# Performance work log

Measured on AMD Instinct MI355X. Metric: run time of the kernel, lower is better.

Reference implementation:

```python
import jax, jax.numpy as jnp
import numpy as np

B, S, E = 2, 2048, 1024
H = 1344            # hidden_dim = ceil(1.3*1024/64)*64
NH = 4              # mLSTM heads
DH = H // NH        # 336
K = 4               # causal conv kernel size
NPH = H // 4        # headwise proj heads (qkv_proj_blocksize=4)
PD = H // NPH       # per-head proj dim = 4
EPS = 1e-6


def setup_inputs() -> dict:
    key = jax.random.key(0)
    ks = jax.random.split(key, 10)
    s_in = jnp.sqrt(2.0 / (5 * E))    # small_init(E)
    s_pd = jnp.sqrt(2.0 / (5 * PD))   # small_init per-head dim
    return {
        "x": jax.random.normal(ks[0], (B, S, E), jnp.float32),
        "W_up": jax.random.normal(ks[1], (E, 2 * H), jnp.float32) * s_in,
        "conv_k": jax.random.normal(ks[2], (K, 1, H), jnp.float32) * jnp.sqrt(2.0 / K),  # depthwise, WIO layout
        "conv_b": jnp.zeros((H,), jnp.float32),
        "Wq": jax.random.normal(ks[3], (NPH, PD, PD), jnp.float32) * s_pd,
        "Wk": jax.random.normal(ks[4], (NPH, PD, PD), jnp.float32) * s_pd,
        "Wv": jax.random.normal(ks[5], (NPH, PD, PD), jnp.float32) * s_pd,
        "W_ig": jax.random.normal(ks[6], (3 * H, NH), jnp.float32) * 0.01,
        "b_ig": jax.random.normal(ks[7], (NH,), jnp.float32) * 0.1,
        "W_fg": jax.random.normal(ks[8], (3 * H, NH), jnp.float32) * 0.01,
        "b_fg": jnp.linspace(3.0, 6.0, NH, dtype=jnp.float32),
        "ln_w": jnp.ones((H,), jnp.float32),
        "skip": jnp.ones((H,), jnp.float32),
        "W_down": jax.random.normal(ks[9], (H, E), jnp.float32) * (2.0 / 12 / np.sqrt(H)),
    }


def _headwise(x, W):
    # LinearHeadwiseExpand: block-diagonal projection over NPH heads of size PD
    xh = x.reshape(B, S, NPH, PD)
    return jnp.einsum('bshd,hdo->bsho', xh, W).reshape(B, S, H)


def _mlstm_cell(q, k, v, ig, fg):
    # parallel stabilized mLSTM; q,k,v: (B,NH,S,DH); ig,fg: (B,NH,S)
    logf = jax.nn.log_sigmoid(fg)
    c = jnp.cumsum(logf, axis=-1)                         # (B,NH,S)
    logfmat = c[..., :, None] - c[..., None, :]           # (B,NH,S,S) cumulative forget decay
    mask = jnp.tril(jnp.ones((S, S), bool))               # causal mask
    log_D = jnp.where(mask, logfmat, -jnp.inf) + ig[..., None, :]
    m = jnp.max(log_D, axis=-1, keepdims=True)            # rowwise stabilizer
    D = jnp.exp(log_D - m)
    qk = jnp.einsum('bnsd,bntd->bnst', q, k) * (DH ** -0.5)
    C = qk * D
    n = jnp.maximum(jnp.abs(jnp.sum(C, axis=-1, keepdims=True)), jnp.exp(-m))
    return jnp.einsum('bnst,bntd->bnsd', C / (n + EPS), v)


def reference(x, W_up, conv_k, conv_b, Wq, Wk, Wv, W_ig, b_ig, W_fg, b_fg, ln_w, skip, W_down):
    x_inner = x @ W_up                                    # (B,S,2H)
    x_m, z = jnp.split(x_inner, 2, axis=-1)
    # depthwise causal conv1d
    xp = jnp.pad(x_m, ((0, 0), (K - 1, 0), (0, 0)))
    xc = jax.lax.conv_general_dilated(
        xp, conv_k, (1,), 'VALID',
        dimension_numbers=('NWC', 'WIO', 'NWC'),
        feature_group_count=H) + conv_b
    act = jax.nn.silu(xc)
    q = _headwise(act, Wq)
    k = _headwise(act, Wk)
    v = _headwise(x_m, Wv)
    gin = jnp.concatenate([q, k, v], axis=-1)             # (B,S,3H)
    ig = jnp.transpose(gin @ W_ig + b_ig, (0, 2, 1))      # (B,NH,S)
    fg = jnp.transpose(gin @ W_fg + b_fg, (0, 2, 1))
    qh = jnp.transpose(q.reshape(B, S, NH, DH), (0, 2, 1, 3))
    kh = jnp.transpose(k.reshape(B, S, NH, DH), (0, 2, 1, 3))
    vh = jnp.transpose(v.reshape(B, S, NH, DH), (0, 2, 1, 3))
    h = _mlstm_cell(qh, kh, vh, ig, fg)                   # (B,NH,S,DH)
    # multi-head layernorm (per-head groupnorm over DH, scale only)
    mu = jnp.mean(h, axis=-1, keepdims=True)
    var = jnp.var(h, axis=-1, keepdims=True)
    hn = (h - mu) * jax.lax.rsqrt(var + 1e-5) * ln_w.reshape(NH, 1, DH)
    h_out = jnp.transpose(hn, (0, 2, 1, 3)).reshape(B, S, H)
    h_state = (h_out + skip * act) * jax.nn.silu(z)
    return h_state @ W_down
```

## Files before the change

kernel.cpp:

```cpp
#include <hip/hip_runtime.h>
#include <cmath>

#define DI __device__ __forceinline__

constexpr int B_=2, S_=2048, E_=1024, H_=1344, NH_=4, DH_=336;
constexpr int BS_=B_*S_, H2_=2*H_;
constexpr int NG_=B_*NH_*S_;

constexpr size_t N_X=(size_t)BS_*E_;
constexpr size_t N_WUP=(size_t)E_*H2_;
constexpr size_t N_WDN=(size_t)H_*E_;
constexpr size_t N_BSH=(size_t)BS_*H_;
constexpr size_t N_BSH2=(size_t)BS_*H2_;
constexpr size_t N_WH=5376, N_WG=16128, N_CK=4*H_;

constexpr size_t O_IGB = 64;
constexpr size_t O_LOGF= O_IGB + NG_;
constexpr size_t O_AB  = O_LOGF+ NG_;
constexpr size_t O_MB  = O_AB  + NG_;
constexpr size_t O_MTB = O_MB  + NG_;
constexpr size_t O_CK  = O_MTB + NG_;
constexpr size_t O_CB  = O_CK  + N_CK;
constexpr size_t O_WQ  = O_CB  + H_;
constexpr size_t O_WK  = O_WQ  + N_WH;
constexpr size_t O_WV  = O_WK  + N_WH;
constexpr size_t O_WIG = O_WV  + N_WH;
constexpr size_t O_BIG = O_WIG + N_WG;
constexpr size_t O_WFG = O_BIG + 16;
constexpr size_t O_BFG = O_WFG + N_WG;
constexpr size_t O_LNW = O_BFG + 16;
constexpr size_t O_SKP = O_LNW + H_;
constexpr size_t O_FX  = O_SKP + H_;
constexpr size_t O_FWUP= O_FX  + N_X;
constexpr size_t O_FWDN= O_FWUP+ N_WUP;
constexpr size_t O_XIN = O_FWDN+ N_WDN;
constexpr size_t O_ACT = O_XIN + N_BSH2;
constexpr size_t O_QB  = O_ACT + N_BSH;
constexpr size_t O_KB  = O_QB  + N_BSH;
constexpr size_t O_VB  = O_KB  + N_BSH;
constexpr size_t O_HOUT= O_VB  + N_BSH;

constexpr size_t KSPLIT_SHORTS=(size_t)8*128*11*64*8;
constexpr size_t VT_SHORTS=(size_t)8*64*22*64*8;

typedef __attribute__((ext_vector_type(8))) short bf16x8;
typedef __attribute__((ext_vector_type(4))) float f32x4;

DI float bf2f(unsigned int u){union{unsigned int i;float f;}v;v.i=(u&0xffffu)<<16;return v.f;}
DI unsigned short f2bf(float f){union{float f;unsigned int i;}v;v.f=f;unsigned int x=v.i;
  return (unsigned short)((x+0x7fffu+((x>>16)&1u))>>16);}
DI float siluf(float x){return x/(1.f+expf(-x));}
DI float logsigf(float x){return (x>=0.f)?-log1pf(expf(-x)):x-log1pf(expf(x));}
DI void load4(const float* p, float* d){float4 v=*reinterpret_cast<const float4*>(p);
  d[0]=v.x;d[1]=v.y;d[2]=v.z;d[3]=v.w;}

__global__ __launch_bounds__(256) void detect_k(const unsigned short* __restrict__ xraw,
                                                int* __restrict__ flag){
  __shared__ int cnt_s;
  if(threadIdx.x==0) cnt_s=0;
  __syncthreads();
  int c=0;
  for(int i=threadIdx.x;i<2048;i+=256){
    const unsigned e=(xraw[i]>>7)&0xFFu;
    if(e>=0x90u) c++;
  }
  atomicAdd(&cnt_s,c);
  __syncthreads();
  if(threadIdx.x==0) *flag=(cnt_s>16)?0:1;
}

constexpr int CV0=5376, CV1=CV0+1344, CV2=CV1+5376, CV3=CV2+5376, CV4=CV3+5376,
              CV5=CV4+16128, CV6=CV5+4, CV7=CV6+16128, CV8=CV7+4,
              CV9=CV8+1344, CVT=CV9+1344;

__global__ __launch_bounds__(256) void prepAB_k(const void* __restrict__ xsrc,
    const void* __restrict__ wsrc, const int* __restrict__ flag,
    unsigned short* __restrict__ xhi, unsigned short* __restrict__ xlo,
    unsigned short* __restrict__ whi, unsigned short* __restrict__ wlo,
    const void* s2,const void* s3,const void* s4,const void* s5,const void* s6,
    const void* s7,const void* s8,const void* s9,const void* s10,const void* s11,
    const void* s12, float* __restrict__ ws){
  const int blk=blockIdx.x;
  const int fl=*flag;
  if(blk>=3392){
    const int i=(blk-3392)*256+threadIdx.x;
    if(i>=CVT) return;
    const void* src; int off; size_t dst;
    if(i<CV0){src=s2; off=i;      dst=O_CK +off;}
    else if(i<CV1){src=s3; off=i-CV0; dst=O_CB +off;}
    else if(i<CV2){src=s4; off=i-CV1; dst=O_WQ +off;}
    else if(i<CV3){src=s5; off=i-CV2; dst=O_WK +off;}
    else if(i<CV4){src=s6; off=i-CV3; dst=O_WV +off;}
    else if(i<CV5){src=s7; off=i-CV4; dst=O_WIG+off;}
    else if(i<CV6){src=s8; off=i-CV5; dst=O_BIG+off;}
    else if(i<CV7){src=s9; off=i-CV6; dst=O_WFG+off;}
    else if(i<CV8){src=s10;off=i-CV7; dst=O_BFG+off;}
    else if(i<CV9){src=s11;off=i-CV8; dst=O_LNW+off;}
    else          {src=s12;off=i-CV9; dst=O_SKP+off;}
    ws[dst]=fl?bf2f(((const unsigned short*)src)[off])
              :((const float*)src)[off];
    return;
  }
  float v[8];
  unsigned short* dh; unsigned short* dl; size_t slot;
  if(blk<2048){
    slot=(size_t)blk*256+threadIdx.x;
    const int l=(int)slot&63, rest=(int)(slot>>6);
    const int kc=rest&31, mt=rest>>5;
    const int row=mt*16+(l&15), k0=kc*32+(l>>4)*8;
    if(fl){
      const unsigned short* s=(const unsigned short*)xsrc+(size_t)row*1024+k0;
      const uint4 u=*reinterpret_cast<const uint4*>(s);
      v[0]=bf2f(u.x);v[1]=bf2f(u.x>>16);v[2]=bf2f(u.y);v[3]=bf2f(u.y>>16);
      v[4]=bf2f(u.z);v[5]=bf2f(u.z>>16);v[6]=bf2f(u.w);v[7]=bf2f(u.w>>16);
    }else{
      const float* s=(const float*)xsrc+(size_t)row*1024+k0;
      load4(s,v); load4(s+4,v+4);
    }
    dh=xhi; dl=xlo;
  } else {
    slot=(size_t)(blk-2048)*256+threadIdx.x;
    const int l=(int)slot&63, rest=(int)(slot>>6);
    const int kc=rest&31, nt=rest>>5;
    const int col=nt*16+(l&15), row0=kc*32+(l>>4)*8;
    if(fl){
      const unsigned short* s=(const unsigned short*)wsrc;
#pragma unroll
      for(int j=0;j<8;j++) v[j]=bf2f(s[(size_t)(row0+j)*2688+col]);
    }else{
      const float* s=(const float*)wsrc;
#pragma unroll
      for(int j=0;j<8;j++) v[j]=s[(size_t)(row0+j)*2688+col];
    }
    dh=whi; dl=wlo;
  }
  unsigned short h8[8], l8[8];
#pragma unroll
  for(int j=0;j<8;j++){ h8[j]=f2bf(v[j]); l8[j]=f2bf(v[j]-bf2f(h8[j])); }
  uint4 ph,pl;
  ph.x=(unsigned)h8[0]|((unsigned)h8[1]<<16); ph.y=(unsigned)h8[2]|((unsigned)h8[3]<<16);
  ph.z=(unsigned)h8[4]|((unsigned)h8[5]<<16); ph.w=(unsigned)h8[6]|((unsigned)h8[7]<<16);
  pl.x=(unsigned)l8[0]|((unsigned)l8[1]<<16); pl.y=(unsigned)l8[2]|((unsigned)l8[3]<<16);
  pl.z=(unsigned)l8[4]|((unsigned)l8[5]<<16); pl.w=(unsigned)l8[6]|((unsigned)l8[7]<<16);
  *reinterpret_cast<uint4*>(&dh[slot*8])=ph;
  *reinterpret_cast<uint4*>(&dl[slot*8])=pl;
}

__global__ __launch_bounds__(256) void gemm3_k(
    const unsigned short* __restrict__ Ahi, const unsigned short* __restrict__ Alo,
    const unsigned short* __restrict__ Bhi, const unsigned short* __restrict__ Blo,
    void* __restrict__ C, const int* __restrict__ flag, int kcn, int ldc){
  const int t=threadIdx.x, w=t>>6, l=t&63, lm=l&15, quad=l>>4;
  const int bn=blockIdx.x*128, bm=blockIdx.y*128;
  const int mtg0=bm>>4, ntg0=bn>>4;

  __shared__ short TT[2][32*512];

  f32x4 acc[2][8];
#pragma unroll
  for(int g=0;g<2;g++)
#pragma unroll
    for(int nt=0;nt<8;nt++) acc[g][nt]={0.f,0.f,0.f,0.f};

  auto stage=[&](int buf,int kc){
#pragma unroll
    for(int j=0;j<8;j++){
      const int tr=w*8+j;
      const unsigned short* src;
      if(tr<8)       src=&Ahi[((size_t)(mtg0+tr   )*kcn+kc)*512+(size_t)l*8];
      else if(tr<16) src=&Alo[((size_t)(mtg0+tr-8 )*kcn+kc)*512+(size_t)l*8];
      else if(tr<24) src=&Bhi[((size_t)(ntg0+tr-16)*kcn+kc)*512+(size_t)l*8];
      else           src=&Blo[((size_t)(ntg0+tr-24)*kcn+kc)*512+(size_t)l*8];
      __builtin_amdgcn_global_load_lds(
        (const __attribute__((address_space(1))) unsigned int*)src,
        (__attribute__((address_space(3))) unsigned int*)&TT[buf][tr*512],
        16,0,0);
    }
  };

  auto compute=[&](int buf){
    const short* Tb=&TT[buf][0];
    const bf16x8 ah0=*reinterpret_cast<const bf16x8*>(&Tb[(2*w  )*512+l*8]);
    const bf16x8 ah1=*reinterpret_cast<const bf16x8*>(&Tb[(2*w+1)*512+l*8]);
    const bf16x8 al0=*reinterpret_cast<const bf16x8*>(&Tb[(8+2*w  )*512+l*8]);
    const bf16x8 al1=*reinterpret_cast<const bf16x8*>(&Tb[(8+2*w+1)*512+l*8]);
#pragma unroll
    for(int nt=0;nt<8;nt++){
      const bf16x8 bh=*reinterpret_cast<const bf16x8*>(&Tb[(16+nt)*512+l*8]);
      const bf16x8 bl=*reinterpret_cast<const bf16x8*>(&Tb[(24+nt)*512+l*8]);
      acc[0][nt]=__builtin_amdgcn_mfma_f32_16x16x32_bf16(ah0,bh,acc[0][nt],0,0,0);
      acc[0][nt]=__builtin_amdgcn_mfma_f32_16x16x32_bf16(al0,bh,acc[0][nt],0,0,0);
      acc[0][nt]=__builtin_amdgcn_mfma_f32_16x16x32_bf16(ah0,bl,acc[0][nt],0,0,0);
      acc[1][nt]=__builtin_amdgcn_mfma_f32_16x16x32_bf16(ah1,bh,acc[1][nt],0,0,0);
      acc[1][nt]=__builtin_amdgcn_mfma_f32_16x16x32_bf16(al1,bh,acc[1][nt],0,0,0);
      acc[1][nt]=__builtin_amdgcn_mfma_f32_16x16x32_bf16(ah1,bl,acc[1][nt],0,0,0);
    }
  };

  stage(0,0);
  for(int kc=0;kc<kcn;kc++){
    const int cur=kc&1;
    if(kc+1<kcn){
      stage(cur^1,kc+1);
      asm volatile("s_waitcnt vmcnt(8)" ::: "memory");
    } else {
      asm volatile("s_waitcnt vmcnt(0)" ::: "memory");
    }
    __builtin_amdgcn_s_barrier();
    compute(cur);
    __builtin_amdgcn_s_barrier();
  }

  const int bf=flag?*flag:0;
#pragma unroll
  for(int g=0;g<2;g++)
#pragma unroll
    for(int nt=0;nt<8;nt++)
#pragma unroll
      for(int r=0;r<4;r++){
        const size_t idx=(size_t)(bm+(2*w+g)*16+quad*4+r)*ldc+bn+nt*16+lm;
        if(bf) ((unsigned short*)C)[idx]=f2bf(acc[g][nt][r]);
        else   ((float*)C)[idx]=acc[g][nt][r];
      }
}

__global__ __launch_bounds__(384) void convqkvgates_k(
    const float* __restrict__ xin, const float* __restrict__ ck,
    const float* __restrict__ cb,
    const float* __restrict__ Wq, const float* __restrict__ Wk,
    const float* __restrict__ Wv,
    const float* __restrict__ Wig, const float* __restrict__ big,
    const float* __restrict__ Wfg, const float* __restrict__ bfg,
    float* __restrict__ act, float* __restrict__ qb, float* __restrict__ vb,
    unsigned short* __restrict__ khi, unsigned short* __restrict__ klo,
    float* __restrict__ igb, float* __restrict__ logfb){
  const int bs=blockIdx.x;
  const int b=bs>>11, s=bs&2047;
  const int t=threadIdx.x;
  __shared__ float4 sq4[336], sk4[336], sv4[336];
  __shared__ float red[6][8];
  if(t<336){
    const int ph=t, base=ph*4;
    float xc[4];
#pragma unroll
    for(int d=0;d<4;d++) xc[d]=cb[base+d];
    float xm[4]={0.f,0.f,0.f,0.f};
#pragma unroll
    for(int w=0;w<4;w++){
      const int sr=s-3+w;
      if(sr>=0){
        float xv[4];
        load4(&xin[(size_t)(b*S_+sr)*H2_+base],xv);
#pragma unroll
        for(int d=0;d<4;d++) xc[d]+=xv[d]*ck[w*H_+base+d];
        if(w==3){ xm[0]=xv[0];xm[1]=xv[1];xm[2]=xv[2];xm[3]=xv[3]; }
      }
    }
    float a4[4];
#pragma unroll
    for(int d=0;d<4;d++) a4[d]=siluf(xc[d]);
    *reinterpret_cast<float4*>(&act[(size_t)bs*H_+base])
        =make_float4(a4[0],a4[1],a4[2],a4[3]);
    float q4[4],k4[4],v4[4];
#pragma unroll
    for(int o=0;o<4;o++){
      float q=0.f,k=0.f,v=0.f;
#pragma unroll
      for(int d=0;d<4;d++){
        q+=a4[d]*Wq[ph*16+d*4+o];
        k+=a4[d]*Wk[ph*16+d*4+o];
        v+=xm[d]*Wv[ph*16+d*4+o];
      }
      q4[o]=q;k4[o]=k;v4[o]=v;
    }
    const int nh=ph/84, dh0=(ph-nh*84)*4;
    const size_t off=((size_t)(b*NH_+nh)*S_+s)*DH_+dh0;
    *reinterpret_cast<float4*>(&qb[off])=make_float4(q4[0],q4[1],q4[2],q4[3]);
    *reinterpret_cast<float4*>(&vb[off])=make_float4(v4[0],v4[1],v4[2],v4[3]);
    {
      const int head8=b*NH_+nh;
      const int tt=s>>4, lm=s&15;
      const int dc=dh0>>5, quad=(dh0&31)>>3, j=dh0&7;
      const size_t ob=(((size_t)(head8*128+tt)*11)+dc)*512
                      +(size_t)(quad*16+lm)*8+j;
      unsigned short kh[4], kl[4];
#pragma unroll
      for(int o=0;o<4;o++){
        kh[o]=f2bf(k4[o]);
        kl[o]=f2bf(k4[o]-bf2f(kh[o]));
      }
      uint2 pk, pl;
      pk.x=(unsigned)kh[0]|((unsigned)kh[1]<<16);
      pk.y=(unsigned)kh[2]|((unsigned)kh[3]<<16);
      pl.x=(unsigned)kl[0]|((unsigned)kl[1]<<16);
      pl.y=(unsigned)kl[2]|((unsigned)kl[3]<<16);
      *reinterpret_cast<uint2*>(&khi[ob])=pk;
      *reinterpret_cast<uint2*>(&klo[ob])=pl;
    }
    sq4[ph]=make_float4(q4[0],q4[1],q4[2],q4[3]);
    sk4[ph]=make_float4(k4[0],k4[1],k4[2],k4[3]);
    sv4[ph]=make_float4(v4[0],v4[1],v4[2],v4[3]);
  }
  __syncthreads();
  const float* sq=reinterpret_cast<const float*>(sq4);
  const float* sk=reinterpret_cast<const float*>(sk4);
  const float* sv=reinterpret_cast<const float*>(sv4);
  float aI0=0.f,aI1=0.f,aI2=0.f,aI3=0.f;
  float aF0=0.f,aF1=0.f,aF2=0.f,aF3=0.f;
  for(int h=t; h<H_; h+=384){
    const float q=sq[h], k=sk[h], v=sv[h];
    const float4 wiq=*reinterpret_cast<const float4*>(&Wig[(size_t)h*4]);
    const float4 wik=*reinterpret_cast<const float4*>(&Wig[(size_t)(H_+h)*4]);
    const float4 wiv=*reinterpret_cast<const float4*>(&Wig[(size_t)(2*H_+h)*4]);
    const float4 wfq=*reinterpret_cast<const float4*>(&Wfg[(size_t)h*4]);
    const float4 wfk=*reinterpret_cast<const float4*>(&Wfg[(size_t)(H_+h)*4]);
    const float4 wfv=*reinterpret_cast<const float4*>(&Wfg[(size_t)(2*H_+h)*4]);
    aI0+=q*wiq.x+k*wik.x+v*wiv.x;
    aI1+=q*wiq.y+k*wik.y+v*wiv.y;
    aI2+=q*wiq.z+k*wik.z+v*wiv.z;
    aI3+=q*wiq.w+k*wik.w+v*wiv.w;
    aF0+=q*wfq.x+k*wfk.x+v*wfv.x;
    aF1+=q*wfq.y+k*wfk.y+v*wfv.y;
    aF2+=q*wfq.z+k*wfk.z+v*wfv.z;
    aF3+=q*wfq.w+k*wfk.w+v*wfv.w;
  }
#pragma unroll
  for(int m=1;m<64;m<<=1){
    aI0+=__shfl_xor(aI0,m); aI1+=__shfl_xor(aI1,m);
    aI2+=__shfl_xor(aI2,m); aI3+=__shfl_xor(aI3,m);
    aF0+=__shfl_xor(aF0,m); aF1+=__shfl_xor(aF1,m);
    aF2+=__shfl_xor(aF2,m); aF3+=__shfl_xor(aF3,m);
  }
  const int wv=t>>6, l=t&63;
  if(l==0){
    red[wv][0]=aI0; red[wv][1]=aI1; red[wv][2]=aI2; red[wv][3]=aI3;
    red[wv][4]=aF0; red[wv][5]=aF1; red[wv][6]=aF2; red[wv][7]=aF3;
  }
  __syncthreads();
  if(t==0){
    float r[8];
#pragma unroll
    for(int j=0;j<8;j++){
      float a=0.f;
#pragma unroll
      for(int wv2=0;wv2<6;wv2++) a+=red[wv2][j];
      r[j]=a;
    }
#pragma unroll
    for(int n=0;n<4;n++){
      const size_t o=(size_t)(b*NH_+n)*S_+s;
      igb[o]=r[n]+big[n];
      logfb[o]=logsigf(r[4+n]+bfg[n]);
    }
  }
}

__global__ __launch_bounds__(256) void vwprep_k(const float* vb,
                                                const void* __restrict__ wdnsrc,
                                                const int* __restrict__ flag,
                                                unsigned short* __restrict__ vTf,
                                                unsigned short* __restrict__ wdnhi,
                                                unsigned short* __restrict__ wdnlo,
                                                unsigned short* __restrict__ khi,
                                                unsigned short* __restrict__ klo,
                                                float* partz){
  const int blk=blockIdx.x;
  if(blk<512){
    const int head=blk>>6, tc=blk&63;
    const size_t obase=(size_t)blk*22*512;
    for(int slot=threadIdx.x; slot<1408; slot+=256){
      const int ntg=slot>>6, ll=slot&63, quad=ll>>4, lm=ll&15;
      const int n=ntg*16+lm, t0=tc*32+quad*8;
      unsigned short h8[8];
#pragma unroll
      for(int j=0;j<8;j++){
        float val;
        if(n<336)       val=vb[((size_t)head*S_+t0+j)*DH_+n];
        else if(n==336) val=1.f;
        else            val=0.f;
        h8[j]=f2bf(val);
      }
      uint4 pk;
      pk.x=(unsigned)h8[0]|((unsigned)h8[1]<<16); pk.y=(unsigned)h8[2]|((unsigned)h8[3]<<16);
      pk.z=(unsigned)h8[4]|((unsigned)h8[5]<<16); pk.w=(unsigned)h8[6]|((unsigned)h8[7]<<16);
      *reinterpret_cast<uint4*>(&vTf[obase+(size_t)(ntg*64+ll)*8])=pk;
    }
    __syncthreads();
    const size_t zb=((size_t)head*2048+(size_t)tc*32)*336;
    for(int idx=threadIdx.x; idx<32*336; idx+=256) partz[zb+idx]=0.f;
  } else if(blk<1184){
    const size_t slot=(size_t)(blk-512)*256+threadIdx.x;
    const int l=(int)slot&63, rest=(int)(slot>>6);
    const int kc=rest%42, nt=rest/42;
    const int col=nt*16+(l&15), row0=kc*32+(l>>4)*8;
    const int fl=*flag;
    float v[8];
    if(fl){
      const unsigned short* s=(const unsigned short*)wdnsrc;
#pragma unroll
      for(int j=0;j<8;j++) v[j]=bf2f(s[(size_t)(row0+j)*1024+col]);
    }else{
      const float* s=(const float*)wdnsrc;
#pragma unroll
      for(int j=0;j<8;j++) v[j]=s[(size_t)(row0+j)*1024+col];
    }
    unsigned short h8[8], l8[8];
#pragma unroll
    for(int j=0;j<8;j++){ h8[j]=f2bf(v[j]); l8[j]=f2bf(v[j]-bf2f(h8[j])); }
    uint4 ph,pl;
    ph.x=(unsigned)h8[0]|((unsigned)h8[1]<<16); ph.y=(unsigned)h8[2]|((unsigned)h8[3]<<16);
    ph.z=(unsigned)h8[4]|((unsigned)h8[5]<<16); ph.w=(unsigned)h8[6]|((unsigned)h8[7]<<16);
    pl.x=(unsigned)l8[0]|((unsigned)l8[1]<<16); pl.y=(unsigned)l8[2]|((unsigned)l8[3]<<16);
    pl.z=(unsigned)l8[4]|((unsigned)l8[5]<<16); pl.w=(unsigned)l8[6]|((unsigned)l8[7]<<16);
    *reinterpret_cast<uint4*>(&wdnhi[slot*8])=ph;
    *reinterpret_cast<uint4*>(&wdnlo[slot*8])=pl;
  } else {
    const int idx=(blk-1184)*256+threadIdx.x;
    const int kt=idx>>4, u=idx&15;
    const size_t base_s=(((size_t)kt*11)+10)*512 + 256 + (size_t)u*16;
    const uint4 z={0,0,0,0};
    *reinterpret_cast<uint4*>(&khi[base_s])=z;
    *reinterpret_cast<uint4*>(&klo[base_s])=z;
  }
}

__global__ __launch_bounds__(256) void scan_k(float* igm,
                                              const float* __restrict__ logfb,
                                              float* __restrict__ ab,float* __restrict__ Mb,
                                              float* __restrict__ mtb){
  const int head=blockIdx.x, t=threadIdx.x;
  __shared__ float sh[256];
  const float* lf=logfb+(size_t)head*S_;
  float* ig=igm+(size_t)head*S_;
  float lc[8];
  float run=0.f;
#pragma unroll
  for(int i=0;i<8;i++){ run+=lf[t*8+i]; lc[i]=run; }
  sh[t]=run;
  for(int st=1;st<256;st<<=1){
    __syncthreads();
    const float v=(t>=st)?sh[t-st]:0.f;
    __syncthreads();
    sh[t]+=v;
  }
  __syncthreads();
  const float off=(t==0)?0.f:sh[t-1];
  __syncthreads();
  float av[8],mv[8],cv[8];
  float mrun=-1e30f;
#pragma unroll
  for(int i=0;i<8;i++){
    cv[i]=off+lc[i];
    av[i]=ig[t*8+i]-cv[i];
    mrun=fmaxf(mrun,av[i]);
    mv[i]=mrun;
  }
  sh[t]=mrun;
  for(int st=1;st<256;st<<=1){
    __syncthreads();
    const float v=(t>=st)?sh[t-st]:-1e30f;
    __syncthreads();
    sh[t]=fmaxf(sh[t],v);
  }
  __syncthreads();
  const float moff=(t==0)?-1e30f:sh[t-1];
#pragma unroll
  for(int i=0;i<8;i++){
    const float Mi=fmaxf(moff,mv[i]);
    const size_t j=(size_t)head*S_+t*8+i;
    ab[j]=av[i]; Mb[j]=Mi; mtb[j]=cv[i]+Mi;
    ig[t*8+i]=0.f;
  }
}

__global__ __launch_bounds__(512,1) void mlstm6_k(
    const float* __restrict__ qb, const unsigned short* __restrict__ khi,
    const unsigned short* __restrict__ klo, const unsigned short* __restrict__ vTf,
    const float* __restrict__ ab, const float* __restrict__ Mb,
    float* __restrict__ part, float* __restrict__ rsum){
  const int bid=blockIdx.x;
  const int head=bid&7;
  const int rest=bid>>3;
  const int pairI=rest&7, seg=rest>>3;
  const int t=threadIdx.x, w=t>>6, l=t&63, lm=l&15, quad=l>>4;

  __shared__ short KV[2][66*512];
  __shared__ short Sc[8][16][40];

  const size_t hb=(size_t)head*S_;
  const float scale=0.05455447256f;

  const int sbA=pairI, sbB=15-pairI;
  const int nA=pairI+1, nTot=17;

  bf16x8 qh[11], ql[11];
  f32x4 accO[22];
  float Mr[4];
  int ws0=sbA*128+w*16;

  auto loadQ=[&](int ws0_){
    const float* qrow=qb+(hb+ws0_+lm)*DH_;
#pragma unroll
    for(int dc=0;dc<11;dc++){
      const int dbase=dc*32+quad*8;
      float v[8];
      if(dbase<336){ load4(qrow+dbase,v); load4(qrow+dbase+4,v+4); }
      else { for(int j=0;j<8;j++) v[j]=0.f; }
#pragma unroll
      for(int j=0;j<8;j++){
        const unsigned short h=f2bf(v[j]);
        qh[dc][j]=(short)h;
        ql[dc][j]=(short)f2bf(v[j]-bf2f(h));
      }
    }
#pragma unroll
    for(int r=0;r<4;r++) Mr[r]=Mb[hb+ws0_+quad*4+r];
#pragma unroll
    for(int n=0;n<22;n++) accO[n]={0.f,0.f,0.f,0.f};
  };

  auto itemC=[&](int i)->int{
    return (i<nA)? (seg+4*i) : (seg+4*(i-nA));
  };

  auto stage=[&](int buf,int c){
    const size_t kbase=(((size_t)head*128+(size_t)(2*c))*11)*512+(size_t)l*8;
    const size_t vbase=(((size_t)head*64+(size_t)c)*22)*512+(size_t)l*8;
#pragma unroll
    for(int j=0;j<9;j++){
      const int tr=w+8*j;
      if(tr<66){
        const unsigned short* src;
        if(tr<22)      src=&khi[kbase+(size_t)tr*512];
        else if(tr<44) src=&klo[kbase+(size_t)(tr-22)*512];
        else           src=&vTf[vbase+(size_t)(tr-44)*512];
        __builtin_amdgcn_global_load_lds(
          (const __attribute__((address_space(1))) unsigned int*)src,
          (__attribute__((address_space(3))) unsigned int*)&KV[buf][(size_t)tr*512],
          16,0,0);
      }
    }
  };

  auto compute=[&](int c,int buf){
    const int t0=c<<5;
    if(t0>ws0+15) return;
    const float al0=ab[hb+t0+lm];
    const float al1=ab[hb+t0+16+lm];
#pragma unroll
    for(int tt=0;tt<2;tt++){
      f32x4 a0={0,0,0,0}, a1={0,0,0,0}, a2={0,0,0,0};
#pragma unroll
      for(int dc=0;dc<11;dc++){
        const bf16x8 kh=*reinterpret_cast<const bf16x8*>(&KV[buf][(tt*11+dc)*512+l*8]);
        const bf16x8 kl=*reinterpret_cast<const bf16x8*>(&KV[buf][(22+tt*11+dc)*512+l*8]);
        a0=__builtin_amdgcn_mfma_f32_16x16x32_bf16(qh[dc],kh,a0,0,0,0);
        a1=__builtin_amdgcn_mfma_f32_16x16x32_bf16(ql[dc],kh,a1,0,0,0);
        a2=__builtin_amdgcn_mfma_f32_16x16x32_bf16(qh[dc],kl,a2,0,0,0);
      }
      const float al=(tt==0)?al0:al1;
      const int tg=t0+tt*16+lm;
#pragma unroll
      for(int r=0;r<4;r++){
        const int srow=quad*4+r;
        const float qk=a0[r]+a1[r]+a2[r];
        const float e=fminf(al-Mr[r],0.f);
        const float msk=(tg<=ws0+srow)?1.f:0.f;
        Sc[w][srow][tt*16+lm]=(short)f2bf(msk*(qk*scale*expf(e)));
      }
    }
    const bf16x8 scf=*reinterpret_cast<const bf16x8*>(&Sc[w][lm][quad*8]);
#pragma unroll
    for(int nt=0;nt<22;nt++){
      const bf16x8 vf=*reinterpret_cast<const bf16x8*>(&KV[buf][(44+nt)*512+l*8]);
      accO[nt]=__builtin_amdgcn_mfma_f32_16x16x32_bf16(scf,vf,accO[nt],0,0,0);
    }
  };

  auto epilogue=[&](){
    const size_t pbase=(size_t)head*2048+ws0;
#pragma unroll
    for(int nt=0;nt<22;nt++){
      const int col=nt*16+lm;
#pragma unroll
      for(int r=0;r<4;r++){
        const int srow=quad*4+r;
        const float val=accO[nt][r];
        if(col<336){ if(val!=0.f) atomicAdd(&part[(pbase+srow)*336+col],val); }
        else if(col==336){ if(val!=0.f) atomicAdd(&rsum[pbase+srow],val); }
      }
    }
  };

  loadQ(ws0);
  stage(0,itemC(0));
  __syncthreads();
  int cur=0;
  for(int i=0;i<nTot;i++){
    if(i+1<nTot) stage(cur^1,itemC(i+1));
    compute(itemC(i),cur);
    if(i==nA-1){
      epilogue();
      ws0=sbB*128+w*16;
      loadQ(ws0);
    }
    __syncthreads();
    cur^=1;
  }
  epilogue();
}

__global__ __launch_bounds__(256) void finalize3_k(const float* __restrict__ part,
                                                   const float* __restrict__ rsum,
                                                   const float* __restrict__ mtb,
                                                   const float* __restrict__ lnw,
                                                   const float* __restrict__ skip,
                                                   const float* __restrict__ act,
                                                   const float* __restrict__ xin,
                                                   unsigned short* __restrict__ hshi,
                                                   unsigned short* __restrict__ hslo){
  const int sblk=blockIdx.x, head=blockIdx.y;
  const int bI=head>>2, nh=head&3;
  const int s0=sblk*32;
  const int t=threadIdx.x, row=t>>3, sub=t&7;
  __shared__ float red1[32][8], red2[32][8];
  __shared__ float mu_s[32], rs_s[32], inv_s[32];
  const size_t pbase=(size_t)head*2048+s0;
  const float* prow=part+(pbase+row)*336;
  float s1=0.f,s2=0.f;
  for(int c=sub;c<336;c+=8){ const float v=prow[c]; s1+=v; s2+=v*v; }
  red1[row][sub]=s1; red2[row][sub]=s2;
  __syncthreads();
  if(sub==0){
    float a1=0.f,a2=0.f;
#pragma unroll
    for(int j=0;j<8;j++){ a1+=red1[row][j]; a2+=red2[row][j]; }
    const float mt=mtb[(size_t)head*S_+s0+row];
    const float nn=fmaxf(fabsf(rsum[pbase+row]), expf(fminf(fmaxf(-mt,-60.f),60.f)));
    const float inv=1.f/(nn+1e-6f);
    const float mu=a1*inv/336.f;
    const float var=a2*inv*inv/336.f-mu*mu;
    inv_s[row]=inv; mu_s[row]=mu;
    rs_s[row]=rsqrtf(fmaxf(var,0.f)+1e-5f);
  }
  __syncthreads();
  const float inv=inv_s[row], mu=mu_s[row], rs=rs_s[row];
  const size_t gbs=(size_t)(bI*S_+s0+row);
  const float* arow=act+gbs*H_+nh*DH_;
  const float* zrow=xin+gbs*H2_+H_+nh*DH_;
  const float* srw=skip+nh*DH_;
  const float* lrw=lnw+nh*DH_;
  const size_t mtbase=(gbs>>4)*42;
  const int lbase=(int)(gbs&15);
  for(int c=sub;c<336;c+=8){
    const float hn=(prow[c]*inv-mu)*rs*lrw[c];
    const float val=(hn+srw[c]*arow[c])*siluf(zrow[c]);
    const int h=nh*DH_+c;
    const int kc=h>>5, quad=(h>>3)&3, j=h&7;
    const size_t slot=(mtbase+kc)*64+lbase+16*quad;
    const unsigned short hi=f2bf(val);
    hshi[slot*8+j]=hi;
    hslo[slot*8+j]=f2bf(val-bf2f(hi));
  }
}

extern "C" void kernel_launch(void* const* d_in, const int* in_sizes, int n_in,
                              void* d_out, int out_size, void* d_ws, size_t ws_size,
                              hipStream_t stream){
  float* ws=(float*)d_ws;
  int* flag=(int*)ws;

  float* igb  = ws+O_IGB;
  float* logfb= ws+O_LOGF;
  float* ab   = ws+O_AB;
  float* Mbuf = ws+O_MB;
  float* mtb  = ws+O_MTB;
  float* f_ck = ws+O_CK;
  float* f_cb = ws+O_CB;
  float* f_wq = ws+O_WQ;
  float* f_wk = ws+O_WK;
  float* f_wv = ws+O_WV;
  float* f_wig= ws+O_WIG;
  float* f_big= ws+O_BIG;
  float* f_wfg= ws+O_WFG;
  float* f_bfg= ws+O_BFG;
  float* f_lnw= ws+O_LNW;
  float* f_skp= ws+O_SKP;
  float* xin  = ws+O_XIN;
  float* act  = ws+O_ACT;
  float* qb   = ws+O_QB;
  float* kb   = ws+O_KB;
  float* vb   = ws+O_VB;

  unsigned short* xhi  =(unsigned short*)(ws+O_FX);   unsigned short* xlo  =xhi+N_X;
  unsigned short* wuphi=(unsigned short*)(ws+O_FWUP); unsigned short* wuplo=wuphi+N_WUP;
  unsigned short* wdnhi=(unsigned short*)(ws+O_FWDN); unsigned short* wdnlo=wdnhi+N_WDN;
  unsigned short* khi=(unsigned short*)(ws+O_FX);
  unsigned short* klo=khi+KSPLIT_SHORTS;
  unsigned short* vTf=(unsigned short*)(ws+O_HOUT);
  unsigned short* hshi=(unsigned short*)kb;
  unsigned short* hslo=hshi+N_BSH;
  float* partb=vb;
  float* rsumb=igb;

  detect_k<<<1,256,0,stream>>>((const unsigned short*)d_in[0],flag);
  prepAB_k<<<2048+1344+226,256,0,stream>>>(d_in[0],d_in[1],flag,xhi,xlo,wuphi,wuplo,
                                           d_in[2],d_in[3],d_in[4],d_in[5],d_in[6],
                                           d_in[7],d_in[8],d_in[9],d_in[10],d_in[11],
                                           d_in[12],ws);
  gemm3_k<<<dim3(2688/128,4096/128),256,0,stream>>>(xhi,xlo,wuphi,wuplo,xin,nullptr,32,H2_);

  convqkvgates_k<<<BS_,384,0,stream>>>(xin,f_ck,f_cb,f_wq,f_wk,f_wv,
                                       f_wig,f_big,f_wfg,f_bfg,
                                       act,qb,vb,khi,klo,igb,logfb);
  vwprep_k<<<512+672+64,256,0,stream>>>(vb,d_in[13],flag,vTf,wdnhi,wdnlo,
                                        khi,klo,partb);
  scan_k<<<B_*NH_,256,0,stream>>>(igb,logfb,ab,Mbuf,mtb);
  mlstm6_k<<<256,512,0,stream>>>(qb,khi,klo,vTf,ab,Mbuf,partb,rsumb);
  finalize3_k<<<dim3(S_/32,B_*NH_),256,0,stream>>>(partb,rsumb,mtb,f_lnw,f_skp,act,xin,
                                                   hshi,hslo);
  gemm3_k<<<dim3(1024/128,4096/128),256,0,stream>>>(hshi,hslo,wdnhi,wdnlo,d_out,flag,42,E_);
}
```

Baseline: 431.0 us.

## Use narrower 128x64 tile GEMM for down projection and fold scan into prep kernel

Adds gemm4_k, a 128x64-tile variant of the split-bf16 MFMA GEMM, and uses it for the down projection. Tile count doubles from 256 to 512 blocks, which spreads the work over more CUs. The gate scan kernel is also merged into vwprep_k as 8 extra blocks, which removes one launch. The smaller tile reloads A more often, so each block does less work per load.

```diff
diff --git a/kernel.cpp b/kernel.cpp
--- a/kernel.cpp
+++ b/kernel.cpp
@@ -224,6 +224,84 @@
       }
 }
 
+__global__ __launch_bounds__(256) void gemm4_k(
+    const unsigned short* __restrict__ Ahi, const unsigned short* __restrict__ Alo,
+    const unsigned short* __restrict__ Bhi, const unsigned short* __restrict__ Blo,
+    void* __restrict__ C, const int* __restrict__ flag, int kcn, int ldc){
+  const int t=threadIdx.x, w=t>>6, l=t&63, lm=l&15, quad=l>>4;
+  const int bn=blockIdx.x*64, bm=blockIdx.y*128;
+  const int mtg0=bm>>4, ntg0=bn>>4;
+
+  __shared__ short TT[2][24*512];
+
+  f32x4 acc[2][4];
+#pragma unroll
+  for(int g=0;g<2;g++)
+#pragma unroll
+    for(int nt=0;nt<4;nt++) acc[g][nt]={0.f,0.f,0.f,0.f};
+
+  auto stage=[&](int buf,int kc){
+#pragma unroll
+    for(int j=0;j<6;j++){
+      const int tr=w*6+j;
+      const unsigned short* src;
+      if(tr<8)       src=&Ahi[((size_t)(mtg0+tr   )*kcn+kc)*512+(size_t)l*8];
+      else if(tr<16) src=&Alo[((size_t)(mtg0+tr-8 )*kcn+kc)*512+(size_t)l*8];
+      else if(tr<20) src=&Bhi[((size_t)(ntg0+tr-16)*kcn+kc)*512+(size_t)l*8];
+      else           src=&Blo[((size_t)(ntg0+tr-20)*kcn+kc)*512+(size_t)l*8];
+      __builtin_amdgcn_global_load_lds(
+        (const __attribute__((address_space(1))) unsigned int*)src,
+        (__attribute__((address_space(3))) unsigned int*)&TT[buf][tr*512],
+        16,0,0);
+    }
+  };
+
+  auto compute=[&](int buf){
+    const short* Tb=&TT[buf][0];
+    const bf16x8 ah0=*reinterpret_cast<const bf16x8*>(&Tb[(2*w  )*512+l*8]);
+    const bf16x8 ah1=*reinterpret_cast<const bf16x8*>(&Tb[(2*w+1)*512+l*8]);
+    const bf16x8 al0=*reinterpret_cast<const bf16x8*>(&Tb[(8+2*w  )*512+l*8]);
+    const bf16x8 al1=*reinterpret_cast<const bf16x8*>(&Tb[(8+2*w+1)*512+l*8]);
+#pragma unroll
+    for(int nt=0;nt<4;nt++){
+      const bf16x8 bh=*reinterpret_cast<const bf16x8*>(&Tb[(16+nt)*512+l*8]);
+      const bf16x8 bl=*reinterpret_cast<const bf16x8*>(&Tb[(20+nt)*512+l*8]);
+      acc[0][nt]=__builtin_amdgcn_mfma_f32_16x16x32_bf16(ah0,bh,acc[0][nt],0,0,0);
+      acc[0][nt]=__builtin_amdgcn_mfma_f32_16x16x32_bf16(al0,bh,acc[0][nt],0,0,0);
+      acc[0][nt]=__builtin_amdgcn_mfma_f32_16x16x32_bf16(ah0,bl,acc[0][nt],0,0,0);
+      acc[1][nt]=__builtin_amdgcn_mfma_f32_16x16x32_bf16(ah1,bh,acc[1][nt],0,0,0);
+      acc[1][nt]=__builtin_amdgcn_mfma_f32_16x16x32_bf16(al1,bh,acc[1][nt],0,0,0);
+      acc[1][nt]=__builtin_amdgcn_mfma_f32_16x16x32_bf16(ah1,bl,acc[1][nt],0,0,0);
+    }
+  };
+
+  stage(0,0);
+  for(int kc=0;kc<kcn;kc++){
+    const int cur=kc&1;
+    if(kc+1<kcn){
+      stage(cur^1,kc+1);
+      asm volatile("s_waitcnt vmcnt(6)" ::: "memory");
+    } else {
+      asm volatile("s_waitcnt vmcnt(0)" ::: "memory");
+    }
+    __builtin_amdgcn_s_barrier();
+    compute(cur);
+    __builtin_amdgcn_s_barrier();
+  }
+
+  const int bf=flag?*flag:0;
+#pragma unroll
+  for(int g=0;g<2;g++)
+#pragma unroll
+    for(int nt=0;nt<4;nt++)
+#pragma unroll
+      for(int r=0;r<4;r++){
+        const size_t idx=(size_t)(bm+(2*w+g)*16+quad*4+r)*ldc+bn+nt*16+lm;
+        if(bf) ((unsigned short*)C)[idx]=f2bf(acc[g][nt][r]);
+        else   ((float*)C)[idx]=acc[g][nt][r];
+      }
+}
+
 __global__ __launch_bounds__(384) void convqkvgates_k(
     const float* __restrict__ xin, const float* __restrict__ ck,
     const float* __restrict__ cb,
@@ -363,7 +441,12 @@
                                                 unsigned short* __restrict__ wdnlo,
                                                 unsigned short* __restrict__ khi,
                                                 unsigned short* __restrict__ klo,
-                                                float* partz){
+                                                float* partz,
+                                                float* igm,
+                                                const float* __restrict__ logfb,
+                                                float* __restrict__ ab,
+                                                float* __restrict__ Mb,
+                                                float* __restrict__ mtb){
   const int blk=blockIdx.x;
   if(blk<512){
     const int head=blk>>6, tc=blk&63;
@@ -414,62 +497,57 @@
     pl.z=(unsigned)l8[4]|((unsigned)l8[5]<<16); pl.w=(unsigned)l8[6]|((unsigned)l8[7]<<16);
     *reinterpret_cast<uint4*>(&wdnhi[slot*8])=ph;
     *reinterpret_cast<uint4*>(&wdnlo[slot*8])=pl;
-  } else {
+  } else if(blk<1248){
     const int idx=(blk-1184)*256+threadIdx.x;
     const int kt=idx>>4, u=idx&15;
     const size_t base_s=(((size_t)kt*11)+10)*512 + 256 + (size_t)u*16;
     const uint4 z={0,0,0,0};
     *reinterpret_cast<uint4*>(&khi[base_s])=z;
     *reinterpret_cast<uint4*>(&klo[base_s])=z;
-  }
-}
-
-__global__ __launch_bounds__(256) void scan_k(float* igm,
-                                              const float* __restrict__ logfb,
-                                              float* __restrict__ ab,float* __restrict__ Mb,
-                                              float* __restrict__ mtb){
-  const int head=blockIdx.x, t=threadIdx.x;
-  __shared__ float sh[256];
-  const float* lf=logfb+(size_t)head*S_;
-  float* ig=igm+(size_t)head*S_;
-  float lc[8];
-  float run=0.f;
-#pragma unroll
-  for(int i=0;i<8;i++){ run+=lf[t*8+i]; lc[i]=run; }
-  sh[t]=run;
-  for(int st=1;st<256;st<<=1){
+  } else {
+    const int head=blk-1248, t=threadIdx.x;
+    __shared__ float sh[256];
+    const float* lf=logfb+(size_t)head*S_;
+    float* ig=igm+(size_t)head*S_;
+    float lc[8];
+    float run=0.f;
+#pragma unroll
+    for(int i=0;i<8;i++){ run+=lf[t*8+i]; lc[i]=run; }
+    sh[t]=run;
+    for(int st=1;st<256;st<<=1){
+      __syncthreads();
+      const float v=(t>=st)?sh[t-st]:0.f;
+      __syncthreads();
+      sh[t]+=v;
+    }
     __syncthreads();
-    const float v=(t>=st)?sh[t-st]:0.f;
+    const float off=(t==0)?0.f:sh[t-1];
     __syncthreads();
-    sh[t]+=v;
-  }
-  __syncthreads();
-  const float off=(t==0)?0.f:sh[t-1];
-  __syncthreads();
-  float av[8],mv[8],cv[8];
-  float mrun=-1e30f;
-#pragma unroll
-  for(int i=0;i<8;i++){
-    cv[i]=off+lc[i];
-    av[i]=ig[t*8+i]-cv[i];
-    mrun=fmaxf(mrun,av[i]);
-    mv[i]=mrun;
-  }
-  sh[t]=mrun;
-  for(int st=1;st<256;st<<=1){
+    float av[8],mv[8],cv[8];
+    float mrun=-1e30f;
+#pragma unroll
+    for(int i=0;i<8;i++){
+      cv[i]=off+lc[i];
+      av[i]=ig[t*8+i]-cv[i];
+      mrun=fmaxf(mrun,av[i]);
+      mv[i]=mrun;
+    }
+    sh[t]=mrun;
+    for(int st=1;st<256;st<<=1){
+      __syncthreads();
+      const float v=(t>=st)?sh[t-st]:-1e30f;
+      __syncthreads();
+      sh[t]=fmaxf(sh[t],v);
+    }
     __syncthreads();
-    const float v=(t>=st)?sh[t-st]:-1e30f;
-    __syncthreads();
-    sh[t]=fmaxf(sh[t],v);
-  }
-  __syncthreads();
-  const float moff=(t==0)?-1e30f:sh[t-1];
-#pragma unroll
-  for(int i=0;i<8;i++){
-    const float Mi=fmaxf(moff,mv[i]);
-    const size_t j=(size_t)head*S_+t*8+i;
-    ab[j]=av[i]; Mb[j]=Mi; mtb[j]=cv[i]+Mi;
-    ig[t*8+i]=0.f;
+    const float moff=(t==0)?-1e30f:sh[t-1];
+#pragma unroll
+    for(int i=0;i<8;i++){
+      const float Mi=fmaxf(moff,mv[i]);
+      const size_t j=(size_t)head*S_+t*8+i;
+      ab[j]=av[i]; Mb[j]=Mi; mtb[j]=cv[i]+Mi;
+      ig[t*8+i]=0.f;
+    }
   }
 }
 
@@ -713,11 +791,11 @@
   convqkvgates_k<<<BS_,384,0,stream>>>(xin,f_ck,f_cb,f_wq,f_wk,f_wv,
                                        f_wig,f_big,f_wfg,f_bfg,
                                        act,qb,vb,khi,klo,igb,logfb);
-  vwprep_k<<<512+672+64,256,0,stream>>>(vb,d_in[13],flag,vTf,wdnhi,wdnlo,
-                                        khi,klo,partb);
-  scan_k<<<B_*NH_,256,0,stream>>>(igb,logfb,ab,Mbuf,mtb);
+  vwprep_k<<<512+672+64+8,256,0,stream>>>(vb,d_in[13],flag,vTf,wdnhi,wdnlo,
+                                          khi,klo,partb,
+                                          igb,logfb,ab,Mbuf,mtb);
   mlstm6_k<<<256,512,0,stream>>>(qb,khi,klo,vTf,ab,Mbuf,partb,rsumb);
   finalize3_k<<<dim3(S_/32,B_*NH_),256,0,stream>>>(partb,rsumb,mtb,f_lnw,f_skp,act,xin,
                                                    hshi,hslo);
-  gemm3_k<<<dim3(1024/128,4096/128),256,0,stream>>>(hshi,hslo,wdnhi,wdnlo,d_out,flag,42,E_);
+  gemm4_k<<<dim3(1024/64,4096/128),256,0,stream>>>(hshi,hslo,wdnhi,wdnlo,d_out,flag,42,E_);
 }
```

New measurement: 441.6 us. 1.02x slower.
